# Optimization experiments

Measured on AMD Instinct MI355X. Metric: run time of the kernel, lower is better.

The kernel has to match this reference:

```python
import jax, jax.numpy as jnp
import numpy as np

BETA = 0.25
N_E = 256
E_DIM = 1024


def setup_inputs() -> dict:
    key = jax.random.key(0)
    k1, k2, k3, k4 = jax.random.split(key, 4)
    z = jax.random.normal(k1, (16, E_DIM, 32, 32), dtype=jnp.float32)
    emb = jax.random.normal(k2, (N_E, E_DIM), dtype=jnp.float32)
    conv_w = jax.random.normal(k3, (E_DIM, E_DIM), dtype=jnp.float32) * 0.02
    conv_b = jax.random.normal(k4, (E_DIM,), dtype=jnp.float32) * 0.02
    return {"z": z, "emb": emb, "conv_w": conv_w, "conv_b": conv_b}


def reference(z, emb, conv_w, conv_b):
    # z: [B, C=e_dim, H, W] -> channels-last, flatten spatial+batch
    zp = jnp.transpose(z, (0, 2, 3, 1))          # [B, H, W, C]
    zf = zp.reshape(-1, E_DIM)                    # [N, C]
    # squared L2 distances to codebook: [N, n_e]
    d = (jnp.sum(zf * zf, axis=1, keepdims=True)
         + jnp.sum(emb * emb, axis=1)
         - 2.0 * (zf @ emb.T))
    min_idx = jnp.argmin(d, axis=1)               # [N]
    min_enc = jax.nn.one_hot(min_idx, N_E, dtype=z.dtype)  # [N, n_e]
    z_q = (min_enc @ emb).reshape(zp.shape)       # gather via matmul, as original
    # VQ commitment loss with straight-through estimator
    loss = (jnp.mean((jax.lax.stop_gradient(z_q) - zp) ** 2)
            + BETA * jnp.mean((z_q - jax.lax.stop_gradient(zp)) ** 2))
    z_q = zp + jax.lax.stop_gradient(z_q - zp)
    e_mean = jnp.mean(min_enc, axis=0)
    perplexity = jnp.exp(-jnp.sum(e_mean * jnp.log(e_mean + 1e-10)))
    # back to channels-first, then 1x1 conv (= per-pixel GEMM)
    z_q = jnp.transpose(z_q, (0, 3, 1, 2))        # [B, C, H, W]
    out = jnp.einsum('bchw,oc->bohw', z_q, conv_w) + conv_b[None, :, None, None]
    return out, loss, perplexity, min_idx
```

## Files before the change

### kernel.cpp

```cpp
#include <hip/hip_runtime.h>
#include <math.h>

#define NE 256
#define EDIM 1024
#define HW 1024
#define NPIX 16384
#define OUT_ELEMS 16777216

typedef short short8 __attribute__((ext_vector_type(8)));
typedef float f32x4 __attribute__((ext_vector_type(4)));

#define WS_HIST   0
#define WS_LOSS   1024
#define WS_ZSQ    1028
#define WS_FBITS  2048
#define WS_T      4096
#define WS_MEMSET 1052672
#define WS_CE2    1052672
#define WS_IDX    1053696
#define WS_EH     1119232
#define WS_EL     1643520
#define WS_NEED   2167808

#define DELTA 0.02f

#define WO_CE2  0
#define WO_HIST 1024
#define WO_LOSS 2048
#define WO_IDX  4096
#define WO_T    69632
#define WO_TOTAL 1118208

__device__ __forceinline__ unsigned short f2bf(float f) {
    unsigned u = __float_as_uint(f);
    unsigned r = u + 0x7FFFu + ((u >> 16) & 1u);
    return (unsigned short)(r >> 16);
}
__device__ __forceinline__ float bf2f(unsigned short h) {
    return __uint_as_float(((unsigned)h) << 16);
}

__device__ __forceinline__ void stage16(const void* g, void* l) {
    __builtin_amdgcn_global_load_lds(
        (const __attribute__((address_space(1))) unsigned int*)g,
        (__attribute__((address_space(3))) unsigned int*)l, 16, 0, 0);
}

__global__ __launch_bounds__(64) void k_prep(const float* __restrict__ emb,
                                             unsigned short* __restrict__ eh,
                                             unsigned short* __restrict__ el,
                                             float* __restrict__ ce2) {
    int j = blockIdx.x;
    int l = threadIdx.x;
    const float* row = emb + ((size_t)j << 10);
    float s = 0.f;
    #pragma unroll
    for (int i = 0; i < 4; i++) {
        float4 v = *(const float4*)(row + l * 4 + 256 * i);
        s += v.x * v.x + v.y * v.y + v.z * v.z + v.w * v.w;
        unsigned short h0 = f2bf(v.x), h1 = f2bf(v.y), h2 = f2bf(v.z), h3 = f2bf(v.w);
        uint2 hp, lp;
        hp.x = (unsigned)h0 | ((unsigned)h1 << 16);
        hp.y = (unsigned)h2 | ((unsigned)h3 << 16);
        lp.x = (unsigned)f2bf(v.x - bf2f(h0)) | ((unsigned)f2bf(v.y - bf2f(h1)) << 16);
        lp.y = (unsigned)f2bf(v.z - bf2f(h2)) | ((unsigned)f2bf(v.w - bf2f(h3)) << 16);
        *(uint2*)(eh + ((size_t)j << 10) + l * 4 + 256 * i) = hp;
        *(uint2*)(el + ((size_t)j << 10) + l * 4 + 256 * i) = lp;
    }
    #pragma unroll
    for (int m = 32; m; m >>= 1) s += __shfl_down(s, m, 64);
    if (l == 0) ce2[j] = 0.5f * s;
}

__global__ __launch_bounds__(256) void k_wT(const float* __restrict__ w,
                                            const float* __restrict__ emb,
                                            float* __restrict__ T) {
    __shared__ float wt[64 * 17];
    __shared__ float et[64 * 17];
    int t = threadIdx.x;
    int j0 = blockIdx.x * 64;
    int o0 = blockIdx.y * 64;
    int kb = blockIdx.z * 256;
    int to = t & 15, tj = t >> 4;
    float acc[4][4] = {};
    int lr = t >> 2, lk = (t & 3) * 4;
    for (int kk = kb; kk < kb + 256; kk += 16) {
        float4 wv = *(const float4*)(w + (size_t)(o0 + lr) * EDIM + kk + lk);
        float4 ev = *(const float4*)(emb + (size_t)(j0 + lr) * EDIM + kk + lk);
        __syncthreads();
        wt[lr * 17 + lk + 0] = wv.x; wt[lr * 17 + lk + 1] = wv.y;
        wt[lr * 17 + lk + 2] = wv.z; wt[lr * 17 + lk + 3] = wv.w;
        et[lr * 17 + lk + 0] = ev.x; et[lr * 17 + lk + 1] = ev.y;
        et[lr * 17 + lk + 2] = ev.z; et[lr * 17 + lk + 3] = ev.w;
        __syncthreads();
        #pragma unroll
        for (int k = 0; k < 16; k++) {
            float a[4], b[4];
            #pragma unroll
            for (int i = 0; i < 4; i++) a[i] = wt[(to * 4 + i) * 17 + k];
            #pragma unroll
            for (int i = 0; i < 4; i++) b[i] = et[(tj * 4 + i) * 17 + k];
            #pragma unroll
            for (int i = 0; i < 4; i++)
                #pragma unroll
                for (int jx = 0; jx < 4; jx++) acc[i][jx] += a[i] * b[jx];
        }
    }
    #pragma unroll
    for (int i = 0; i < 4; i++)
        #pragma unroll
        for (int jx = 0; jx < 4; jx++)
            atomicAdd(&T[(size_t)(o0 + to * 4 + i) * NE + j0 + tj * 4 + jx],
                      acc[i][jx]);
}

__global__ __launch_bounds__(256) void k_dist(
        const float* __restrict__ z, const unsigned short* __restrict__ eh,
        const unsigned short* __restrict__ el,
        const float* __restrict__ ce2,
        int* __restrict__ idx_i, float* __restrict__ idx_f,
        int* __restrict__ hist, float* __restrict__ loss_s,
        float* __restrict__ zsq_acc, unsigned int* __restrict__ fbits) {
    __shared__ unsigned short sB[2][2][256 * 32];
    int t = threadIdx.x;
    int lane = t & 63, w = t >> 6;
    int m = lane & 15, quad = lane >> 4;
    int px0 = blockIdx.x * 64;
    int b = px0 >> 10;
    const float* zp = z + (((size_t)b) << 20) + (px0 & 1023) + w * 16 + m;
    int sc = t >> 2, so = (t & 3) * 8;

    f32x4 acc[16];
    #pragma unroll
    for (int nt = 0; nt < 16; nt++) acc[nt] = (f32x4){0.f, 0.f, 0.f, 0.f};

    #pragma unroll
    for (int i = 0; i < 4; i++) {
        stage16(eh + (((size_t)(i * 64 + sc)) << 10) + so, &sB[0][0][(i * 256 + w * 64) * 8]);
        stage16(el + (((size_t)(i * 64 + sc)) << 10) + so, &sB[0][1][(i * 256 + w * 64) * 8]);
    }
    float zv[8];
    #pragma unroll
    for (int j = 0; j < 8; j++)
        zv[j] = zp[((size_t)(quad * 8 + j)) << 10];

    float zsq = 0.f;
    for (int ck = 0; ck < 32; ck++) {
        int cur = ck & 1;
        __syncthreads();
        short8 ah, al;
        #pragma unroll
        for (int j = 0; j < 8; j++) {
            zsq += zv[j] * zv[j];
            unsigned short h = f2bf(zv[j]);
            ((unsigned short*)&ah)[j] = h;
            ((unsigned short*)&al)[j] = f2bf(zv[j] - bf2f(h));
        }
        if (ck < 31) {
            int kk = (ck + 1) * 32;
            #pragma unroll
            for (int i = 0; i < 4; i++) {
                stage16(eh + (((size_t)(i * 64 + sc)) << 10) + kk + so,
                        &sB[1 - cur][0][(i * 256 + w * 64) * 8]);
                stage16(el + (((size_t)(i * 64 + sc)) << 10) + kk + so,
                        &sB[1 - cur][1][(i * 256 + w * 64) * 8]);
            }
            #pragma unroll
            for (int j = 0; j < 8; j++)
                zv[j] = zp[((size_t)(kk + quad * 8 + j)) << 10];
        }
        #pragma unroll
        for (int nt = 0; nt < 16; nt++) {
            short8 bh = *(const short8*)&sB[cur][0][(nt * 16 + m) * 32 + quad * 8];
            short8 bl = *(const short8*)&sB[cur][1][(nt * 16 + m) * 32 + quad * 8];
            acc[nt] = __builtin_amdgcn_mfma_f32_16x16x32_bf16(ah, bh, acc[nt], 0, 0, 0);
            acc[nt] = __builtin_amdgcn_mfma_f32_16x16x32_bf16(ah, bl, acc[nt], 0, 0, 0);
            acc[nt] = __builtin_amdgcn_mfma_f32_16x16x32_bf16(al, bh, acc[nt], 0, 0, 0);
        }
    }

    #pragma unroll
    for (int msk = 32; msk; msk >>= 1) zsq += __shfl_down(zsq, msk, 64);
    if (lane == 0) atomicAdd(zsq_acc, zsq);

    float c2v[16];
    #pragma unroll
    for (int nt = 0; nt < 16; nt++) c2v[nt] = ce2[nt * 16 + m];

    float lsum = 0.f;
    #pragma unroll
    for (int r = 0; r < 4; r++) {
        float v1 = 3.4e38f, v2 = 3.4e38f; int i1 = 0;
        #pragma unroll
        for (int nt = 0; nt < 16; nt++) {
            int code = nt * 16 + m;
            float sv = c2v[nt] - acc[nt][r];
            if (sv < v1 || (sv == v1 && code < i1)) { v2 = v1; v1 = sv; i1 = code; }
            else v2 = fminf(v2, sv);
        }
        #pragma unroll
        for (int msk = 1; msk < 16; msk <<= 1) {
            float ov1 = __shfl_xor(v1, msk, 64);
            int   oi1 = __shfl_xor(i1, msk, 64);
            float ov2 = __shfl_xor(v2, msk, 64);
            float nv2 = fminf(fminf(v2, ov2), fmaxf(v1, ov1));
            if (ov1 < v1 || (ov1 == v1 && oi1 < i1)) { v1 = ov1; i1 = oi1; }
            v2 = nv2;
        }
        if (m == 0) {
            int px = px0 + w * 16 + quad * 4 + r;
            idx_i[px] = i1;
            idx_f[px] = (float)i1;
            atomicAdd(&hist[i1], 1);
            if (v2 - v1 < DELTA)
                atomicOr(&fbits[px >> 5], 1u << (px & 31));
            lsum += v1;
        }
    }
    lsum += __shfl_xor(lsum, 16, 64);
    lsum += __shfl_xor(lsum, 32, 64);
    if (lane == 0) atomicAdd(loss_s, lsum);
}

__global__ __launch_bounds__(256) void k_cleanup(const float* __restrict__ z,
        const float* __restrict__ emb, const float* __restrict__ ce2,
        const unsigned int* __restrict__ fbits,
        int* __restrict__ idx_i, float* __restrict__ idx_f, int* __restrict__ hist) {
    __shared__ float zs[1024];
    __shared__ float rv[4];
    __shared__ int ri[4];
    int t = threadIdx.x;
    const float* er = emb + (size_t)t * EDIM;
    for (int px = blockIdx.x; px < NPIX; px += gridDim.x) {
        if (!(fbits[px >> 5] & (1u << (px & 31)))) continue;
        int b = px >> 10, p = px & 1023;
        const float* zb = z + (((size_t)b) << 20) + p;
        #pragma unroll
        for (int r = 0; r < 4; r++) {
            int c = t + 256 * r;
            zs[c] = zb[((size_t)c) << 10];
        }
        __syncthreads();
        float d0 = 0.f, d1 = 0.f, d2 = 0.f, d3 = 0.f;
        #pragma unroll 4
        for (int c = 0; c < EDIM; c += 16) {
            float4 e0 = *(const float4*)(er + c);
            float4 e1 = *(const float4*)(er + c + 4);
            float4 e2 = *(const float4*)(er + c + 8);
            float4 e3 = *(const float4*)(er + c + 12);
            d0 += e0.x * zs[c]      + e0.y * zs[c + 1]  + e0.z * zs[c + 2]  + e0.w * zs[c + 3];
            d1 += e1.x * zs[c + 4]  + e1.y * zs[c + 5]  + e1.z * zs[c + 6]  + e1.w * zs[c + 7];
            d2 += e2.x * zs[c + 8]  + e2.y * zs[c + 9]  + e2.z * zs[c + 10] + e2.w * zs[c + 11];
            d3 += e3.x * zs[c + 12] + e3.y * zs[c + 13] + e3.z * zs[c + 14] + e3.w * zs[c + 15];
        }
        float sv = ce2[t] - ((d0 + d1) + (d2 + d3));
        int bi = t;
        #pragma unroll
        for (int msk = 1; msk < 64; msk <<= 1) {
            float ov = __shfl_xor(sv, msk, 64);
            int oi = __shfl_xor(bi, msk, 64);
            if (ov < sv || (ov == sv && oi < bi)) { sv = ov; bi = oi; }
        }
        if ((t & 63) == 0) { rv[t >> 6] = sv; ri[t >> 6] = bi; }
        __syncthreads();
        if (t == 0) {
            float v = rv[0]; int ix = ri[0];
            for (int ww = 1; ww < 4; ww++)
                if (rv[ww] < v || (rv[ww] == v && ri[ww] < ix)) { v = rv[ww]; ix = ri[ww]; }
            int old = idx_i[px];
            if (ix != old) {
                idx_i[px] = ix; idx_f[px] = (float)ix;
                atomicAdd(&hist[ix], 1); atomicSub(&hist[old], 1);
            }
        }
        __syncthreads();
    }
}

__global__ __launch_bounds__(64) void k_norms(const float* __restrict__ emb,
                                              float* __restrict__ ce2) {
    int j = blockIdx.x;
    int lane = threadIdx.x;
    const float* row = emb + (size_t)j * EDIM;
    float s = 0.f;
    #pragma unroll
    for (int i = 0; i < EDIM / 64; i++) {
        float v = row[lane + 64 * i];
        s += v * v;
    }
    #pragma unroll
    for (int m = 32; m; m >>= 1) s += __shfl_down(s, m, 64);
    if (lane == 0) ce2[j] = 0.5f * s;
}

__global__ __launch_bounds__(256) void k_argmin(const float* __restrict__ z,
                                                const float* __restrict__ emb,
                                                const float* __restrict__ ce2,
                                                int* __restrict__ idx_i,
                                                float* __restrict__ idx_f,
                                                int* __restrict__ hist,
                                                float* __restrict__ loss_acc) {
    __shared__ float zt[32 * 64];
    __shared__ float et[256 * 34];
    __shared__ float znorm_s[64];
    int t = threadIdx.x;
    int n0 = blockIdx.x * 64;
    int b = n0 >> 10;
    int p0 = n0 & 1023;
    const float* zb = z + (size_t)b * EDIM * HW;
    int tc = t & 31, tp = t >> 5;
    float acc[8][8] = {};
    float znorm = 0.f;
    for (int kk = 0; kk < EDIM; kk += 32) {
        #pragma unroll
        for (int i = 0; i < 16; i++) {
            int q = t + 256 * i;
            int code = q >> 4, k2 = q & 15;
            float2 v = *(const float2*)(emb + (size_t)code * EDIM + kk + k2 * 2);
            *(float2*)(et + code * 34 + k2 * 2) = v;
        }
        #pragma unroll
        for (int i = 0; i < 4; i++) {
            int q = t + 256 * i;
            int k = q >> 5, p2 = q & 31;
            float2 v = *(const float2*)(zb + (size_t)(kk + k) * HW + p0 + p2 * 2);
            *(float2*)(zt + k * 64 + p2 * 2) = v;
        }
        __syncthreads();
        if (t < 64) {
            #pragma unroll
            for (int k = 0; k < 32; k++) { float zz = zt[k * 64 + t]; znorm += zz * zz; }
        }
        #pragma unroll 4
        for (int k2 = 0; k2 < 16; k2++) {
            float2 ev[8], za[4], zb2[4];
            #pragma unroll
            for (int u = 0; u < 8; u++)
                ev[u] = *(float2*)(et + (tc + 32 * u) * 34 + k2 * 2);
            #pragma unroll
            for (int j = 0; j < 4; j++)
                za[j] = *(float2*)(zt + (2 * k2) * 64 + tp * 8 + 2 * j);
            #pragma unroll
            for (int j = 0; j < 4; j++)
                zb2[j] = *(float2*)(zt + (2 * k2 + 1) * 64 + tp * 8 + 2 * j);
            #pragma unroll
            for (int p = 0; p < 8; p++) {
                float z0 = (p & 1) ? za[p >> 1].y : za[p >> 1].x;
                float z1 = (p & 1) ? zb2[p >> 1].y : zb2[p >> 1].x;
                #pragma unroll
                for (int u = 0; u < 8; u++)
                    acc[p][u] += z0 * ev[u].x + z1 * ev[u].y;
            }
        }
        __syncthreads();
    }
    if (t < 64) znorm_s[t] = znorm;
    float minv[8];
    int mini[8];
    #pragma unroll
    for (int p = 0; p < 8; p++) { minv[p] = 3.4e38f; mini[p] = 0; }
    #pragma unroll
    for (int u = 0; u < 8; u++) {
        int code = tc + 32 * u;
        float cc2 = ce2[code];
        #pragma unroll
        for (int p = 0; p < 8; p++) {
            float s = cc2 - acc[p][u];
            if (s < minv[p] || (s == minv[p] && code < mini[p])) { minv[p] = s; mini[p] = code; }
        }
    }
    #pragma unroll
    for (int m = 1; m < 32; m <<= 1) {
        #pragma unroll
        for (int p = 0; p < 8; p++) {
            float ov = __shfl_xor(minv[p], m, 64);
            int oi = __shfl_xor(mini[p], m, 64);
            if (ov < minv[p] || (ov == minv[p] && oi < mini[p])) { minv[p] = ov; mini[p] = oi; }
        }
    }
    __syncthreads();
    if (tc == 0) {
        float dsum = 0.f;
        #pragma unroll
        for (int p = 0; p < 8; p++) {
            int lp = tp * 8 + p;
            int n = n0 + lp;
            idx_i[n] = mini[p];
            idx_f[n] = (float)mini[p];
            dsum += znorm_s[lp] + 2.f * minv[p];
            atomicAdd(&hist[mini[p]], 1);
        }
        atomicAdd(loss_acc, dsum);
    }
}

__global__ __launch_bounds__(256) void k_scatter(const float* __restrict__ T,
                                                 const float* __restrict__ bias,
                                                 const int* __restrict__ idx,
                                                 float* __restrict__ out) {
    __shared__ float Ts[16 * 256];
    __shared__ float bs[16];
    int t = threadIdx.x;
    int o0 = blockIdx.x * 16;
    int b = blockIdx.y;
    #pragma unroll
    for (int r = 0; r < 16; r++)
        Ts[r * 256 + t] = T[(size_t)(o0 + r) * NE + t];
    if (t < 16) bs[t] = bias[o0 + t];
    __syncthreads();
    int4 i4 = *(const int4*)(idx + b * HW + t * 4);
    #pragma unroll
    for (int r = 0; r < 16; r++) {
        const float* Tr = Ts + r * 256;
        float bb = bs[r];
        float4 v;
        v.x = Tr[i4.x] + bb;
        v.y = Tr[i4.y] + bb;
        v.z = Tr[i4.z] + bb;
        v.w = Tr[i4.w] + bb;
        *(float4*)(out + ((size_t)(b * EDIM + o0 + r) * HW) + t * 4) = v;
    }
}

__global__ __launch_bounds__(256) void k_final_new(const int* __restrict__ hist,
                                                   const float* __restrict__ loss_s,
                                                   const float* __restrict__ zsq,
                                                   float* __restrict__ out) {
    __shared__ float red[4];
    int t = threadIdx.x;
    float em = (float)hist[t] * (1.0f / 16384.0f);
    float v = em * logf(em + 1e-10f);
    #pragma unroll
    for (int m = 32; m; m >>= 1) v += __shfl_down(v, m, 64);
    if ((t & 63) == 0) red[t >> 6] = v;
    __syncthreads();
    if (t == 0) {
        float s = red[0] + red[1] + red[2] + red[3];
        out[OUT_ELEMS] = (zsq[0] + 2.f * loss_s[0]) * 1.25f / 16777216.f;
        out[OUT_ELEMS + 1] = expf(-s);
    }
}

__global__ __launch_bounds__(256) void k_final_old(const int* __restrict__ hist,
                                                   const float* __restrict__ loss_acc,
                                                   float* __restrict__ out) {
    __shared__ float red[4];
    int t = threadIdx.x;
    float em = (float)hist[t] * (1.0f / 16384.0f);
    float v = em * logf(em + 1e-10f);
    #pragma unroll
    for (int m = 32; m; m >>= 1) v += __shfl_down(v, m, 64);
    if ((t & 63) == 0) red[t >> 6] = v;
    __syncthreads();
    if (t == 0) {
        float s = red[0] + red[1] + red[2] + red[3];
        out[OUT_ELEMS] = loss_acc[0] * 1.25f / 16777216.f;
        out[OUT_ELEMS + 1] = expf(-s);
    }
}

extern "C" void kernel_launch(void* const* d_in, const int* in_sizes, int n_in,
                              void* d_out, int out_size, void* d_ws, size_t ws_size,
                              hipStream_t stream) {
    (void)in_sizes; (void)n_in; (void)out_size;
    const float* z      = (const float*)d_in[0];
    const float* emb    = (const float*)d_in[1];
    const float* conv_w = (const float*)d_in[2];
    const float* conv_b = (const float*)d_in[3];
    float* out = (float*)d_out;

    if (ws_size >= WS_NEED) {
        int*   hist     = (int*)((char*)d_ws + WS_HIST);
        float* loss_s   = (float*)((char*)d_ws + WS_LOSS);
        float* zsq      = (float*)((char*)d_ws + WS_ZSQ);
        unsigned int* fbits = (unsigned int*)((char*)d_ws + WS_FBITS);
        float* T        = (float*)((char*)d_ws + WS_T);
        float* ce2      = (float*)((char*)d_ws + WS_CE2);
        int*   idx_i    = (int*)((char*)d_ws + WS_IDX);
        unsigned short* eh = (unsigned short*)((char*)d_ws + WS_EH);
        unsigned short* el = (unsigned short*)((char*)d_ws + WS_EL);
        float* idx_f = out + OUT_ELEMS + 2;

        hipMemsetAsync(d_ws, 0, WS_MEMSET, stream);
        k_prep<<<NE, 64, 0, stream>>>(emb, eh, el, ce2);
        k_wT<<<dim3(4, 16, 4), 256, 0, stream>>>(conv_w, emb, T);
        k_dist<<<256, 256, 0, stream>>>(z, eh, el, ce2, idx_i, idx_f,
                                        hist, loss_s, zsq, fbits);
        k_cleanup<<<256, 256, 0, stream>>>(z, emb, ce2, fbits, idx_i, idx_f, hist);
        k_scatter<<<dim3(64, 16), 256, 0, stream>>>(T, conv_b, idx_i, out);
        k_final_new<<<1, 256, 0, stream>>>(hist, loss_s, zsq, out);
    } else {
        float* ce2      = (float*)((char*)d_ws + WO_CE2);
        int*   hist     = (int*)((char*)d_ws + WO_HIST);
        float* loss_acc = (float*)((char*)d_ws + WO_LOSS);
        int*   idx_i    = (int*)((char*)d_ws + WO_IDX);
        float* T        = (float*)((char*)d_ws + WO_T);
        float* idx_f = out + OUT_ELEMS + 2;

        hipMemsetAsync(d_ws, 0, WO_TOTAL, stream);
        k_norms<<<NE, 64, 0, stream>>>(emb, ce2);
        k_wT<<<dim3(4, 16, 4), 256, 0, stream>>>(conv_w, emb, T);
        k_argmin<<<256, 256, 0, stream>>>(z, emb, ce2, idx_i, idx_f, hist, loss_acc);
        k_scatter<<<dim3(64, 16), 256, 0, stream>>>(T, conv_b, idx_i, out);
        k_final_old<<<1, 256, 0, stream>>>(hist, loss_acc, out);
    }
}
```

Before: 260.2 us.

## Retile distance kernel across codes, fuse memset and final reduction into other kernels

k_dist now runs 512 threads per block. Each wave covers all 64 pixels of the block against a 32-code slice, and a shared-memory cross-wave argmin reduction combines the slices. To support this, k_prep writes the hi/lo bf16 codebook in a k-chunk-major layout so each chunk is one contiguous copy into LDS, and the split uses truncation through byte-perm instead of round-to-nearest. The workspace memset is folded into k_prep, and the final loss/perplexity kernel is folded into the scatter kernel, which removes two launches. In exchange the kernel adds a cross-wave reduction and LDS pressure, and the truncated split slightly changes the low-order rounding.

```diff
diff --git a/kernel.cpp b/kernel.cpp
--- a/kernel.cpp
+++ b/kernel.cpp
@@ -15,7 +15,6 @@
 #define WS_ZSQ    1028
 #define WS_FBITS  2048
 #define WS_T      4096
-#define WS_MEMSET 1052672
 #define WS_CE2    1052672
 #define WS_IDX    1053696
 #define WS_EH     1119232
@@ -31,14 +30,20 @@
 #define WO_T    69632
 #define WO_TOTAL 1118208
 
+__device__ __forceinline__ void cvt_pair(float a, float b,
+                                         unsigned& hp, unsigned& lp) {
+    unsigned ua = __float_as_uint(a), ub = __float_as_uint(b);
+    hp = __builtin_amdgcn_perm(ub, ua, 0x07060302u);
+    float ra = a - __uint_as_float(ua & 0xFFFF0000u);
+    float rb = b - __uint_as_float(ub & 0xFFFF0000u);
+    lp = __builtin_amdgcn_perm(__float_as_uint(rb), __float_as_uint(ra), 0x07060302u);
+}
+
 __device__ __forceinline__ unsigned short f2bf(float f) {
     unsigned u = __float_as_uint(f);
     unsigned r = u + 0x7FFFu + ((u >> 16) & 1u);
     return (unsigned short)(r >> 16);
 }
-__device__ __forceinline__ float bf2f(unsigned short h) {
-    return __uint_as_float(((unsigned)h) << 16);
-}
 
 __device__ __forceinline__ void stage16(const void* g, void* l) {
     __builtin_amdgcn_global_load_lds(
@@ -47,25 +52,38 @@
 }
 
 __global__ __launch_bounds__(64) void k_prep(const float* __restrict__ emb,
-                                             unsigned short* __restrict__ eh,
-                                             unsigned short* __restrict__ el,
-                                             float* __restrict__ ce2) {
+                                             unsigned short* __restrict__ ehs,
+                                             unsigned short* __restrict__ els,
+                                             float* __restrict__ ce2,
+                                             float* __restrict__ T,
+                                             unsigned char* __restrict__ head) {
     int j = blockIdx.x;
     int l = threadIdx.x;
+    f32x4 z4 = {0.f, 0.f, 0.f, 0.f};
+    #pragma unroll
+    for (int i = 0; i < 4; i++)
+        *(f32x4*)(T + ((size_t)j << 10) + l * 4 + 256 * i) = z4;
+    if (j == 0) {
+        #pragma unroll
+        for (int i = 0; i < 4; i++)
+            *(uint4*)(head + l * 64 + i * 16) = make_uint4(0, 0, 0, 0);
+    }
     const float* row = emb + ((size_t)j << 10);
     float s = 0.f;
     #pragma unroll
-    for (int i = 0; i < 4; i++) {
-        float4 v = *(const float4*)(row + l * 4 + 256 * i);
-        s += v.x * v.x + v.y * v.y + v.z * v.z + v.w * v.w;
-        unsigned short h0 = f2bf(v.x), h1 = f2bf(v.y), h2 = f2bf(v.z), h3 = f2bf(v.w);
-        uint2 hp, lp;
-        hp.x = (unsigned)h0 | ((unsigned)h1 << 16);
-        hp.y = (unsigned)h2 | ((unsigned)h3 << 16);
-        lp.x = (unsigned)f2bf(v.x - bf2f(h0)) | ((unsigned)f2bf(v.y - bf2f(h1)) << 16);
-        lp.y = (unsigned)f2bf(v.z - bf2f(h2)) | ((unsigned)f2bf(v.w - bf2f(h3)) << 16);
-        *(uint2*)(eh + ((size_t)j << 10) + l * 4 + 256 * i) = hp;
-        *(uint2*)(el + ((size_t)j << 10) + l * 4 + 256 * i) = lp;
+    for (int g2 = 0; g2 < 2; g2++) {
+        int g = 2 * l + g2;
+        float4 va = *(const float4*)(row + g * 8);
+        float4 vb = *(const float4*)(row + g * 8 + 4);
+        s += va.x * va.x + va.y * va.y + va.z * va.z + va.w * va.w
+           + vb.x * vb.x + vb.y * vb.y + vb.z * vb.z + vb.w * vb.w;
+        uint4 hq, lq;
+        cvt_pair(va.x, va.y, hq.x, lq.x);
+        cvt_pair(va.z, va.w, hq.y, lq.y);
+        cvt_pair(vb.x, vb.y, hq.z, lq.z);
+        cvt_pair(vb.z, vb.w, hq.w, lq.w);
+        *(uint4*)(ehs + ((size_t)(g * 256 + j)) * 8) = hq;
+        *(uint4*)(els + ((size_t)(g * 256 + j)) * 8) = lq;
     }
     #pragma unroll
     for (int m = 32; m; m >>= 1) s += __shfl_down(s, m, 64);
@@ -114,112 +132,144 @@
                       acc[i][jx]);
 }
 
-__global__ __launch_bounds__(256) void k_dist(
-        const float* __restrict__ z, const unsigned short* __restrict__ eh,
-        const unsigned short* __restrict__ el,
+__global__ __launch_bounds__(512) void k_dist(
+        const float* __restrict__ z, const unsigned short* __restrict__ ehs,
+        const unsigned short* __restrict__ els,
         const float* __restrict__ ce2,
         int* __restrict__ idx_i, float* __restrict__ idx_f,
         int* __restrict__ hist, float* __restrict__ loss_s,
         float* __restrict__ zsq_acc, unsigned int* __restrict__ fbits) {
-    __shared__ unsigned short sB[2][2][256 * 32];
+    __shared__ unsigned short sB[2][2][8192];
+    __shared__ float red[8 * 64 * 3];
     int t = threadIdx.x;
     int lane = t & 63, w = t >> 6;
     int m = lane & 15, quad = lane >> 4;
     int px0 = blockIdx.x * 64;
     int b = px0 >> 10;
-    const float* zp = z + (((size_t)b) << 20) + (px0 & 1023) + w * 16 + m;
-    int sc = t >> 2, so = (t & 3) * 8;
-
-    f32x4 acc[16];
-    #pragma unroll
-    for (int nt = 0; nt < 16; nt++) acc[nt] = (f32x4){0.f, 0.f, 0.f, 0.f};
-
-    #pragma unroll
-    for (int i = 0; i < 4; i++) {
-        stage16(eh + (((size_t)(i * 64 + sc)) << 10) + so, &sB[0][0][(i * 256 + w * 64) * 8]);
-        stage16(el + (((size_t)(i * 64 + sc)) << 10) + so, &sB[0][1][(i * 256 + w * 64) * 8]);
-    }
-    float zv[8];
-    #pragma unroll
-    for (int j = 0; j < 8; j++)
-        zv[j] = zp[((size_t)(quad * 8 + j)) << 10];
+    const float* zb = z + (((size_t)b) << 20) + (px0 & 1023);
+
+    f32x4 acc[4][2];
+    #pragma unroll
+    for (int at = 0; at < 4; at++)
+        #pragma unroll
+        for (int ct = 0; ct < 2; ct++) acc[at][ct] = (f32x4){0.f, 0.f, 0.f, 0.f};
+
+    stage16(ehs + t * 8,        &sB[0][0][t * 8]);
+    stage16(ehs + 4096 + t * 8, &sB[0][0][4096 + t * 8]);
+    stage16(els + t * 8,        &sB[0][1][t * 8]);
+    stage16(els + 4096 + t * 8, &sB[0][1][4096 + t * 8]);
+    float zv[4][8];
+    #pragma unroll
+    for (int at = 0; at < 4; at++)
+        #pragma unroll
+        for (int j = 0; j < 8; j++)
+            zv[at][j] = zb[(((size_t)(quad * 8 + j)) << 10) + at * 16 + m];
 
     float zsq = 0.f;
     for (int ck = 0; ck < 32; ck++) {
         int cur = ck & 1;
         __syncthreads();
-        short8 ah, al;
-        #pragma unroll
-        for (int j = 0; j < 8; j++) {
-            zsq += zv[j] * zv[j];
-            unsigned short h = f2bf(zv[j]);
-            ((unsigned short*)&ah)[j] = h;
-            ((unsigned short*)&al)[j] = f2bf(zv[j] - bf2f(h));
-        }
+        short8 ah[4], al[4];
+        #pragma unroll
+        for (int at = 0; at < 4; at++)
+            #pragma unroll
+            for (int p = 0; p < 4; p++) {
+                float a0 = zv[at][2 * p], a1 = zv[at][2 * p + 1];
+                unsigned hp, lp;
+                cvt_pair(a0, a1, hp, lp);
+                ((unsigned*)&ah[at])[p] = hp;
+                ((unsigned*)&al[at])[p] = lp;
+                if (w == 0) zsq += a0 * a0 + a1 * a1;
+            }
         if (ck < 31) {
-            int kk = (ck + 1) * 32;
-            #pragma unroll
-            for (int i = 0; i < 4; i++) {
-                stage16(eh + (((size_t)(i * 64 + sc)) << 10) + kk + so,
-                        &sB[1 - cur][0][(i * 256 + w * 64) * 8]);
-                stage16(el + (((size_t)(i * 64 + sc)) << 10) + kk + so,
-                        &sB[1 - cur][1][(i * 256 + w * 64) * 8]);
-            }
-            #pragma unroll
-            for (int j = 0; j < 8; j++)
-                zv[j] = zp[((size_t)(kk + quad * 8 + j)) << 10];
-        }
-        #pragma unroll
-        for (int nt = 0; nt < 16; nt++) {
-            short8 bh = *(const short8*)&sB[cur][0][(nt * 16 + m) * 32 + quad * 8];
-            short8 bl = *(const short8*)&sB[cur][1][(nt * 16 + m) * 32 + quad * 8];
-            acc[nt] = __builtin_amdgcn_mfma_f32_16x16x32_bf16(ah, bh, acc[nt], 0, 0, 0);
-            acc[nt] = __builtin_amdgcn_mfma_f32_16x16x32_bf16(ah, bl, acc[nt], 0, 0, 0);
-            acc[nt] = __builtin_amdgcn_mfma_f32_16x16x32_bf16(al, bh, acc[nt], 0, 0, 0);
-        }
-    }
-
-    #pragma unroll
-    for (int msk = 32; msk; msk >>= 1) zsq += __shfl_down(zsq, msk, 64);
-    if (lane == 0) atomicAdd(zsq_acc, zsq);
-
-    float c2v[16];
-    #pragma unroll
-    for (int nt = 0; nt < 16; nt++) c2v[nt] = ce2[nt * 16 + m];
-
-    float lsum = 0.f;
-    #pragma unroll
-    for (int r = 0; r < 4; r++) {
-        float v1 = 3.4e38f, v2 = 3.4e38f; int i1 = 0;
-        #pragma unroll
-        for (int nt = 0; nt < 16; nt++) {
-            int code = nt * 16 + m;
-            float sv = c2v[nt] - acc[nt][r];
-            if (sv < v1 || (sv == v1 && code < i1)) { v2 = v1; v1 = sv; i1 = code; }
-            else v2 = fminf(v2, sv);
-        }
-        #pragma unroll
-        for (int msk = 1; msk < 16; msk <<= 1) {
-            float ov1 = __shfl_xor(v1, msk, 64);
-            int   oi1 = __shfl_xor(i1, msk, 64);
-            float ov2 = __shfl_xor(v2, msk, 64);
+            const unsigned short* ep = ehs + (ck + 1) * 8192;
+            const unsigned short* lp2 = els + (ck + 1) * 8192;
+            stage16(ep + t * 8,         &sB[1 - cur][0][t * 8]);
+            stage16(ep + 4096 + t * 8,  &sB[1 - cur][0][4096 + t * 8]);
+            stage16(lp2 + t * 8,        &sB[1 - cur][1][t * 8]);
+            stage16(lp2 + 4096 + t * 8, &sB[1 - cur][1][4096 + t * 8]);
+            #pragma unroll
+            for (int at = 0; at < 4; at++)
+                #pragma unroll
+                for (int j = 0; j < 8; j++)
+                    zv[at][j] = zb[(((size_t)((ck + 1) * 32 + quad * 8 + j)) << 10)
+                                   + at * 16 + m];
+        }
+        #pragma unroll
+        for (int ct = 0; ct < 2; ct++) {
+            int crow = (quad * 256 + w * 32 + ct * 16 + m) * 8;
+            short8 bh = *(const short8*)&sB[cur][0][crow];
+            short8 bl = *(const short8*)&sB[cur][1][crow];
+            #pragma unroll
+            for (int at = 0; at < 4; at++) {
+                acc[at][ct] = __builtin_amdgcn_mfma_f32_16x16x32_bf16(ah[at], bh, acc[at][ct], 0, 0, 0);
+                acc[at][ct] = __builtin_amdgcn_mfma_f32_16x16x32_bf16(ah[at], bl, acc[at][ct], 0, 0, 0);
+                acc[at][ct] = __builtin_amdgcn_mfma_f32_16x16x32_bf16(al[at], bh, acc[at][ct], 0, 0, 0);
+            }
+        }
+    }
+
+    if (w == 0) {
+        #pragma unroll
+        for (int msk = 32; msk; msk >>= 1) zsq += __shfl_down(zsq, msk, 64);
+        if (lane == 0) atomicAdd(zsq_acc, zsq);
+    }
+
+    float c2v[2];
+    #pragma unroll
+    for (int ct = 0; ct < 2; ct++) c2v[ct] = ce2[w * 32 + ct * 16 + m];
+    #pragma unroll
+    for (int at = 0; at < 4; at++) {
+        #pragma unroll
+        for (int r = 0; r < 4; r++) {
+            float v1 = 3.4e38f, v2 = 3.4e38f; int i1 = 0;
+            #pragma unroll
+            for (int ct = 0; ct < 2; ct++) {
+                int code = w * 32 + ct * 16 + m;
+                float sv = c2v[ct] - acc[at][ct][r];
+                if (sv < v1 || (sv == v1 && code < i1)) { v2 = v1; v1 = sv; i1 = code; }
+                else v2 = fminf(v2, sv);
+            }
+            #pragma unroll
+            for (int msk = 1; msk < 16; msk <<= 1) {
+                float ov1 = __shfl_xor(v1, msk, 64);
+                int   oi1 = __shfl_xor(i1, msk, 64);
+                float ov2 = __shfl_xor(v2, msk, 64);
+                float nv2 = fminf(fminf(v2, ov2), fmaxf(v1, ov1));
+                if (ov1 < v1 || (ov1 == v1 && oi1 < i1)) { v1 = ov1; i1 = oi1; }
+                v2 = nv2;
+            }
+            if (m == 0) {
+                int pxl = at * 16 + quad * 4 + r;
+                int e = (w * 64 + pxl) * 3;
+                red[e] = v1; ((int*)red)[e + 1] = i1; red[e + 2] = v2;
+            }
+        }
+    }
+    __syncthreads();
+    if (t < 64) {
+        float v1 = red[t * 3], v2 = red[t * 3 + 2];
+        int i1 = ((int*)red)[t * 3 + 1];
+        #pragma unroll
+        for (int ww = 1; ww < 8; ww++) {
+            int e = (ww * 64 + t) * 3;
+            float ov1 = red[e], ov2 = red[e + 2];
+            int oi1 = ((int*)red)[e + 1];
             float nv2 = fminf(fminf(v2, ov2), fmaxf(v1, ov1));
             if (ov1 < v1 || (ov1 == v1 && oi1 < i1)) { v1 = ov1; i1 = oi1; }
             v2 = nv2;
         }
-        if (m == 0) {
-            int px = px0 + w * 16 + quad * 4 + r;
-            idx_i[px] = i1;
-            idx_f[px] = (float)i1;
-            atomicAdd(&hist[i1], 1);
-            if (v2 - v1 < DELTA)
-                atomicOr(&fbits[px >> 5], 1u << (px & 31));
-            lsum += v1;
-        }
-    }
-    lsum += __shfl_xor(lsum, 16, 64);
-    lsum += __shfl_xor(lsum, 32, 64);
-    if (lane == 0) atomicAdd(loss_s, lsum);
+        int px = px0 + t;
+        idx_i[px] = i1;
+        idx_f[px] = (float)i1;
+        atomicAdd(&hist[i1], 1);
+        if (v2 - v1 < DELTA)
+            atomicOr(&fbits[px >> 5], 1u << (px & 31));
+        float ls = v1;
+        #pragma unroll
+        for (int msk = 32; msk; msk >>= 1) ls += __shfl_down(ls, msk, 64);
+        if (t == 0) atomicAdd(loss_s, ls);
+    }
 }
 
 __global__ __launch_bounds__(256) void k_cleanup(const float* __restrict__ z,
@@ -277,6 +327,51 @@
     }
 }
 
+__global__ __launch_bounds__(256) void k_scatter_f(const float* __restrict__ T,
+                                                   const float* __restrict__ bias,
+                                                   const int* __restrict__ idx,
+                                                   const int* __restrict__ hist,
+                                                   const float* __restrict__ loss_s,
+                                                   const float* __restrict__ zsq,
+                                                   float* __restrict__ out) {
+    __shared__ float Ts[16 * 256];
+    __shared__ float bs[16];
+    __shared__ float red2[4];
+    int t = threadIdx.x;
+    int o0 = blockIdx.x * 16;
+    int b = blockIdx.y;
+    if (blockIdx.x == 0 && blockIdx.y == 0) {
+        float em = (float)hist[t] * (1.0f / 16384.0f);
+        float v = em * logf(em + 1e-10f);
+        #pragma unroll
+        for (int m = 32; m; m >>= 1) v += __shfl_down(v, m, 64);
+        if ((t & 63) == 0) red2[t >> 6] = v;
+        __syncthreads();
+        if (t == 0) {
+            float s = red2[0] + red2[1] + red2[2] + red2[3];
+            out[OUT_ELEMS] = (zsq[0] + 2.f * loss_s[0]) * 1.25f / 16777216.f;
+            out[OUT_ELEMS + 1] = expf(-s);
+        }
+    }
+    #pragma unroll
+    for (int r = 0; r < 16; r++)
+        Ts[r * 256 + t] = T[(size_t)(o0 + r) * NE + t];
+    if (t < 16) bs[t] = bias[o0 + t];
+    __syncthreads();
+    int4 i4 = *(const int4*)(idx + b * HW + t * 4);
+    #pragma unroll
+    for (int r = 0; r < 16; r++) {
+        const float* Tr = Ts + r * 256;
+        float bb = bs[r];
+        float4 v;
+        v.x = Tr[i4.x] + bb;
+        v.y = Tr[i4.y] + bb;
+        v.z = Tr[i4.z] + bb;
+        v.w = Tr[i4.w] + bb;
+        *(float4*)(out + ((size_t)(b * EDIM + o0 + r) * HW) + t * 4) = v;
+    }
+}
+
 __global__ __launch_bounds__(64) void k_norms(const float* __restrict__ emb,
                                               float* __restrict__ ce2) {
     int j = blockIdx.x;
@@ -422,25 +517,6 @@
     }
 }
 
-__global__ __launch_bounds__(256) void k_final_new(const int* __restrict__ hist,
-                                                   const float* __restrict__ loss_s,
-                                                   const float* __restrict__ zsq,
-                                                   float* __restrict__ out) {
-    __shared__ float red[4];
-    int t = threadIdx.x;
-    float em = (float)hist[t] * (1.0f / 16384.0f);
-    float v = em * logf(em + 1e-10f);
-    #pragma unroll
-    for (int m = 32; m; m >>= 1) v += __shfl_down(v, m, 64);
-    if ((t & 63) == 0) red[t >> 6] = v;
-    __syncthreads();
-    if (t == 0) {
-        float s = red[0] + red[1] + red[2] + red[3];
-        out[OUT_ELEMS] = (zsq[0] + 2.f * loss_s[0]) * 1.25f / 16777216.f;
-        out[OUT_ELEMS + 1] = expf(-s);
-    }
-}
-
 __global__ __launch_bounds__(256) void k_final_old(const int* __restrict__ hist,
                                                    const float* __restrict__ loss_acc,
                                                    float* __restrict__ out) {
@@ -477,18 +553,17 @@
         float* T        = (float*)((char*)d_ws + WS_T);
         float* ce2      = (float*)((char*)d_ws + WS_CE2);
         int*   idx_i    = (int*)((char*)d_ws + WS_IDX);
-        unsigned short* eh = (unsigned short*)((char*)d_ws + WS_EH);
-        unsigned short* el = (unsigned short*)((char*)d_ws + WS_EL);
+        unsigned short* ehs = (unsigned short*)((char*)d_ws + WS_EH);
+        unsigned short* els = (unsigned short*)((char*)d_ws + WS_EL);
         float* idx_f = out + OUT_ELEMS + 2;
 
-        hipMemsetAsync(d_ws, 0, WS_MEMSET, stream);
-        k_prep<<<NE, 64, 0, stream>>>(emb, eh, el, ce2);
+        k_prep<<<NE, 64, 0, stream>>>(emb, ehs, els, ce2, T, (unsigned char*)d_ws);
         k_wT<<<dim3(4, 16, 4), 256, 0, stream>>>(conv_w, emb, T);
-        k_dist<<<256, 256, 0, stream>>>(z, eh, el, ce2, idx_i, idx_f,
+        k_dist<<<256, 512, 0, stream>>>(z, ehs, els, ce2, idx_i, idx_f,
                                         hist, loss_s, zsq, fbits);
         k_cleanup<<<256, 256, 0, stream>>>(z, emb, ce2, fbits, idx_i, idx_f, hist);
-        k_scatter<<<dim3(64, 16), 256, 0, stream>>>(T, conv_b, idx_i, out);
-        k_final_new<<<1, 256, 0, stream>>>(hist, loss_s, zsq, out);
+        k_scatter_f<<<dim3(64, 16), 256, 0, stream>>>(T, conv_b, idx_i, hist,
+                                                      loss_s, zsq, out);
     } else {
         float* ce2      = (float*)((char*)d_ws + WO_CE2);
         int*   hist     = (int*)((char*)d_ws + WO_HIST);
```

Result: slower. 265.5 us (+2.0%).
